# Kernel tuning notes

Measured on AMD Instinct MI355X. Metric: run time of the kernel, lower is better.

## Reference

```python
import jax, jax.numpy as jnp
import numpy as np

# Semantic hierarchy configuration (stand-in for semantic_softmax_processor)
GROUP_SIZES = [8192, 4096, 2048, 1024, 512, 256, 128, 64, 32, 16]
NORM_FACTORS = [0.1] * len(GROUP_SIZES)
TOPK_CAP = 500
TEMPERATURE = 1.0
TOTAL_CLASSES = sum(GROUP_SIZES)  # 16368
BATCH = 1024


def setup_inputs() -> dict:
    key = jax.random.key(0)
    k1, k2, k3 = jax.random.split(key, 3)
    logits = jax.random.normal(k1, (BATCH, TOTAL_CLASSES), dtype=jnp.float32)
    logits_teacher = jax.random.normal(k2, (BATCH, TOTAL_CLASSES), dtype=jnp.float32)
    targets = jax.random.randint(k3, (BATCH,), 0, TOTAL_CLASSES, dtype=jnp.int64)
    return {"logits": logits, "logits_teacher": logits_teacher, "targets": targets}


def _group_kd_loss(s_logits, t_logits, temperature):
    # s_logits, t_logits: [B, C_i] for one semantic group
    B, C = t_logits.shape
    k = min(C, TOPK_CAP)
    # teacher top-k classes (sorted, largest)
    t_top, t_idx = jax.lax.top_k(t_logits, k)                 # [B, k]
    s_top = jnp.take_along_axis(s_logits, t_idx, axis=1)      # [B, k]
    log_p = jax.nn.log_softmax(s_top / temperature, axis=1)   # student log-probs
    log_q = jax.nn.log_softmax(t_top / temperature, axis=1)   # teacher log-probs
    q = jnp.exp(log_q)
    # KL(q || p), reduction='batchmean'
    kl = jnp.sum(q * (log_q - log_p)) / B
    return kl * temperature * temperature


def reference(logits, logits_teacher, targets):
    # targets are converted to semantic targets in the original module but are
    # never used in the loss computation (dead code) -> no effect on output.
    del targets
    total = jnp.float32(0.0)
    offset = 0
    for gsize, norm in zip(GROUP_SIZES, NORM_FACTORS):
        s_i = jax.lax.slice_in_dim(logits, offset, offset + gsize, axis=1)
        t_i = jax.lax.slice_in_dim(logits_teacher, offset, offset + gsize, axis=1)
        total = total + _group_kd_loss(s_i, t_i, TEMPERATURE) * norm
        offset += gsize
    return total
```

## Files before the change

### kernel.cpp

```cpp
#include <hip/hip_runtime.h>
#include <stdint.h>
#include <float.h>

#define TOTAL 16368
#define KSEL 500
#define CAP 1280
#define NSLOT 20
#define HCAP 672
#define NSEG 21
#define NBUCKET 64

__device__ __forceinline__ uint32_t fkey(float f) {
    uint32_t u = __float_as_uint(f);
    return (u & 0x80000000u) ? ~u : (u | 0x80000000u);
}
__device__ __forceinline__ float keyf(uint32_t k) {
    uint32_t u = (k & 0x80000000u) ? (k & 0x7FFFFFFFu) : ~k;
    return __uint_as_float(u);
}
__device__ __forceinline__ int wave_sumi(int v) {
    #pragma unroll
    for (int o = 32; o > 0; o >>= 1) v += __shfl_xor(v, o, 64);
    return v;
}
__device__ __forceinline__ float wave_sumf(float v) {
    #pragma unroll
    for (int o = 32; o > 0; o >>= 1) v += __shfl_xor(v, o, 64);
    return v;
}
__device__ __forceinline__ float wave_maxf(float v) {
    #pragma unroll
    for (int o = 32; o > 0; o >>= 1) v = fmaxf(v, __shfl_xor(v, o, 64));
    return v;
}
__device__ __forceinline__ void lse_merge(float& m, float& l, float m2, float l2) {
    float M = fmaxf(m, m2);
    l = l * __expf(m - M) + l2 * __expf(m2 - M);
    m = M;
}

__device__ __noinline__ float wave_slow_kl(const float* __restrict__ t,
                                           const float* __restrict__ s, int C) {
    const int lane = threadIdx.x & 63;
    uint64_t lo = 0ull, hi = (1ull << 45), tau = 0ull;
    int cl = C, ch = 0;
    for (int it = 0; it < 100; ++it) {
        uint64_t span = hi - lo;
        if (span <= 1ull) { tau = lo; break; }
        uint64_t mid;
        if (it & 1) mid = lo + (span >> 1);
        else {
            uint64_t st = span * (uint64_t)(cl - KSEL) / (uint64_t)(cl - ch);
            if (st < 1) st = 1;
            if (st > span - 1) st = span - 1;
            mid = lo + st;
        }
        int c = 0;
        for (int i = lane; i < C; i += 64) {
            uint64_t ck = ((uint64_t)fkey(t[i]) << 13) | (uint64_t)(8191 - i);
            c += (ck > mid);
        }
        c = wave_sumi(c);
        if (c == KSEL) { tau = mid; break; }
        if (c > KSEL) { lo = mid; cl = c; } else { hi = mid; ch = c; }
    }
    float tmx = -FLT_MAX;
    for (int i = lane; i < C; i += 64) tmx = fmaxf(tmx, t[i]);
    tmx = wave_maxf(tmx);
    float St = 0.f, Stt = 0.f, Sts = 0.f, sm = -FLT_MAX;
    for (int i = lane; i < C; i += 64) {
        float x = t[i];
        uint64_t ck = ((uint64_t)fkey(x) << 13) | (uint64_t)(8191 - i);
        if (ck > tau) {
            float e = __expf(x - tmx), v = s[i];
            St += e; Stt += e * x; Sts += e * v;
            sm = fmaxf(sm, v);
        }
    }
    St = wave_sumf(St); Stt = wave_sumf(Stt); Sts = wave_sumf(Sts); sm = wave_maxf(sm);
    float Ss = 0.f;
    for (int i = lane; i < C; i += 64) {
        uint64_t ck = ((uint64_t)fkey(t[i]) << 13) | (uint64_t)(8191 - i);
        if (ck > tau) Ss += __expf(s[i] - sm);
    }
    Ss = wave_sumf(Ss);
    if (lane == 0)
        return (Stt - Sts) / St - tmx - __logf(St) + sm + __logf(Ss);
    return 0.f;
}

template <int NF4>
__device__ float big_wave(const float* __restrict__ tg, const float* __restrict__ s,
                          float thr, float* vals, uint16_t* idxs) {
    const int lane = threadIdx.x & 63;
    const float4* t4 = (const float4*)tg;
    int cnt = 0;
    #pragma unroll
    for (int c0 = 0; c0 < NF4; c0 += 8) {
        float4 buf[8];
        #pragma unroll
        for (int u = 0; u < 8; ++u) buf[u] = t4[(c0 + u) * 64 + lane];
        int myc = 0;
        #pragma unroll
        for (int u = 0; u < 8; ++u)
            myc += (buf[u].x > thr) + (buf[u].y > thr) +
                   (buf[u].z > thr) + (buf[u].w > thr);
        int inc = myc;
        #pragma unroll
        for (int o = 1; o < 64; o <<= 1) {
            int y = __shfl_up(inc, o, 64);
            if (lane >= o) inc += y;
        }
        int base = cnt + inc - myc;
        cnt += __shfl(inc, 63, 64);
        #pragma unroll
        for (int u = 0; u < 8; ++u) {
            float xs[4] = {buf[u].x, buf[u].y, buf[u].z, buf[u].w};
            #pragma unroll
            for (int q = 0; q < 4; ++q) {
                if (xs[q] > thr) {
                    if (base < CAP) {
                        vals[base] = xs[q];
                        idxs[base] = (uint16_t)((((c0 + u) * 64 + lane) << 2) + q);
                    }
                    ++base;
                }
            }
        }
    }
    if (cnt < KSEL || cnt > CAP) return wave_slow_kl(tg, s, NF4 * 256);

    uint32_t key[NSLOT];
    float svc[NSLOT];
    #pragma unroll
    for (int j = 0; j < NSLOT; ++j) {
        int p = lane + j * 64;
        bool v = p < cnt;
        key[j] = v ? fkey(vals[p]) : 0u;
        svc[j] = v ? s[(int)idxs[p]] : 0.f;
    }
    uint32_t kmx = 0u, kmn = 0xFFFFFFFFu;
    #pragma unroll
    for (int j = 0; j < NSLOT; ++j) {
        uint32_t k = key[j];
        kmx = k > kmx ? k : kmx;
        if (k) kmn = k < kmn ? k : kmn;
    }
    #pragma unroll
    for (int o = 32; o > 0; o >>= 1) {
        uint32_t a = __shfl_xor(kmx, o, 64); kmx = a > kmx ? a : kmx;
        uint32_t b = __shfl_xor(kmn, o, 64); kmn = b < kmn ? b : kmn;
    }
    const float tmax = keyf(kmx);

    uint32_t lo = kmn - 1u, hi = kmx, tauhi = kmx;
    int cl = cnt, ch = 0, cut = -1;
    bool exact = false;
    for (int it = 0; it < 80; ++it) {
        uint32_t span = hi - lo;
        if (span <= 1u) break;
        uint32_t mid;
        if (!(it & 1)) {
            uint64_t st = (uint64_t)span * (uint32_t)(cl - KSEL) / (uint32_t)(cl - ch);
            if (st < 1) st = 1;
            if (st > span - 1) st = span - 1;
            mid = lo + (uint32_t)st;
        } else mid = lo + (span >> 1);
        int c = 0;
        #pragma unroll
        for (int j = 0; j < NSLOT; ++j) c += (key[j] > mid);
        c = wave_sumi(c);
        if (c == KSEL) { tauhi = mid; exact = true; break; }
        if (c > KSEL) { lo = mid; cl = c; } else { hi = mid; ch = c; }
    }
    if (!exact) {
        tauhi = hi;
        const int nT = KSEL - ch, nTie = cl - ch;
        if (nT >= nTie) cut = 0x7FFFFFFF;
        else {
            int l = -1, h = 8191;
            while (h - l > 1) {
                int m = (l + h) >> 1;
                int c = 0;
                #pragma unroll
                for (int j = 0; j < NSLOT; ++j) {
                    int p = lane + j * 64;
                    c += (key[j] == tauhi && p < cnt && (int)idxs[p] <= m);
                }
                c = wave_sumi(c);
                if (c >= nT) h = m; else l = m;
            }
            cut = h;
        }
    }

    uint32_t selm = 0u;
    if (cut == -1) {
        #pragma unroll
        for (int j = 0; j < NSLOT; ++j) selm |= (key[j] > tauhi ? 1u : 0u) << j;
    } else if (cut == 0x7FFFFFFF) {
        #pragma unroll
        for (int j = 0; j < NSLOT; ++j) selm |= (key[j] >= tauhi ? 1u : 0u) << j;
    } else {
        #pragma unroll
        for (int j = 0; j < NSLOT; ++j) {
            int p = lane + j * 64;
            bool sj = (key[j] > tauhi) ||
                      (key[j] == tauhi && p < cnt && (int)idxs[p] <= cut);
            selm |= (sj ? 1u : 0u) << j;
        }
    }

    float St = 0.f, Stt = 0.f, Sts = 0.f, sm = -FLT_MAX;
    #pragma unroll
    for (int j = 0; j < NSLOT; ++j) {
        if (selm & (1u << j)) {
            float tv = keyf(key[j]);
            float e = __expf(tv - tmax);
            St += e; Stt += e * tv; Sts += e * svc[j];
            sm = fmaxf(sm, svc[j]);
        }
    }
    #pragma unroll
    for (int o = 32; o > 0; o >>= 1) {
        St  += __shfl_xor(St,  o, 64);
        Stt += __shfl_xor(Stt, o, 64);
        Sts += __shfl_xor(Sts, o, 64);
        sm = fmaxf(sm, __shfl_xor(sm, o, 64));
    }
    float Ss = 0.f;
    #pragma unroll
    for (int j = 0; j < NSLOT; ++j)
        if (selm & (1u << j)) Ss += __expf(svc[j] - sm);
    Ss = wave_sumf(Ss);
    if (lane == 0)
        return (Stt - Sts) / St - tmax - __logf(St) + sm + __logf(Ss);
    return 0.f;
}

__device__ int half_compact(const float* __restrict__ tq, const float* __restrict__ sg,
                            float thr, int idx_off,
                            uint32_t* kv, float* sv, uint16_t* ix) {
    const int lane = threadIdx.x & 63;
    const float4* t4 = (const float4*)tq;
    int cnt = 0;
    #pragma unroll
    for (int c0 = 0; c0 < 16; c0 += 8) {
        float4 buf[8];
        #pragma unroll
        for (int u = 0; u < 8; ++u) buf[u] = t4[(c0 + u) * 64 + lane];
        int myc = 0;
        #pragma unroll
        for (int u = 0; u < 8; ++u)
            myc += (buf[u].x > thr) + (buf[u].y > thr) +
                   (buf[u].z > thr) + (buf[u].w > thr);
        int inc = myc;
        #pragma unroll
        for (int o = 1; o < 64; o <<= 1) {
            int y = __shfl_up(inc, o, 64);
            if (lane >= o) inc += y;
        }
        int base = cnt + inc - myc;
        cnt += __shfl(inc, 63, 64);
        #pragma unroll
        for (int u = 0; u < 8; ++u) {
            float xs[4] = {buf[u].x, buf[u].y, buf[u].z, buf[u].w};
            #pragma unroll
            for (int q = 0; q < 4; ++q) {
                if (xs[q] > thr) {
                    if (base < HCAP) {
                        kv[base] = fkey(xs[q]);
                        ix[base] = (uint16_t)(((((c0 + u) * 64 + lane) << 2) + q)
                                              + idx_off);
                    }
                    ++base;
                }
            }
        }
    }
    if (cnt <= HCAP) {
        for (int p = cnt + lane; p < HCAP; p += 64) kv[p] = 0u;
        float r[11];
        #pragma unroll
        for (int j = 0; j < 11; ++j) {
            int p = lane + j * 64;
            r[j] = (p < cnt) ? sg[(int)ix[p]] : 0.f;
        }
        #pragma unroll
        for (int j = 0; j < 11; ++j) {
            int p = lane + j * 64;
            if (p < cnt) sv[p] = r[j];
        }
    }
    return cnt;
}

__device__ float pair_select(const uint32_t* __restrict__ kv,
                             const float* __restrict__ sv,
                             const uint16_t* __restrict__ ix,
                             const int* cnts,
                             const float* __restrict__ tg,
                             const float* __restrict__ sg) {
    const int lane = threadIdx.x & 63;
    const int tot = cnts[0] + cnts[1];
    bool bad = (tot < KSEL) || (cnts[0] > HCAP) || (cnts[1] > HCAP);
    if (bad) return wave_slow_kl(tg, sg, 8192);

    uint32_t key[NSEG];
    #pragma unroll
    for (int j = 0; j < NSEG; ++j) key[j] = kv[lane + j * 64];

    uint32_t kmx = 0u, kmn = 0xFFFFFFFFu;
    #pragma unroll
    for (int j = 0; j < NSEG; ++j) {
        uint32_t k = key[j];
        kmx = k > kmx ? k : kmx;
        if (k) kmn = k < kmn ? k : kmn;
    }
    #pragma unroll
    for (int o = 32; o > 0; o >>= 1) {
        uint32_t a = __shfl_xor(kmx, o, 64); kmx = a > kmx ? a : kmx;
        uint32_t b = __shfl_xor(kmn, o, 64); kmn = b < kmn ? b : kmn;
    }
    const float tmax = keyf(kmx);

    uint32_t lo = kmn - 1u, hi = kmx, tauhi = kmx;
    int cl = tot, ch = 0, cut = -1;
    bool exact = false;
    for (int it = 0; it < 80; ++it) {
        uint32_t span = hi - lo;
        if (span <= 1u) break;
        uint32_t mid;
        if (!(it & 1)) {
            uint64_t st = (uint64_t)span * (uint32_t)(cl - KSEL) / (uint32_t)(cl - ch);
            if (st < 1) st = 1;
            if (st > span - 1) st = span - 1;
            mid = lo + (uint32_t)st;
        } else mid = lo + (span >> 1);
        int c = 0;
        #pragma unroll
        for (int j = 0; j < NSEG; ++j) c += (key[j] > mid);
        c = wave_sumi(c);
        if (c == KSEL) { tauhi = mid; exact = true; break; }
        if (c > KSEL) { lo = mid; cl = c; } else { hi = mid; ch = c; }
    }
    if (!exact) {
        tauhi = hi;
        const int nT = KSEL - ch, nTie = cl - ch;
        if (nT >= nTie) cut = 0x7FFFFFFF;
        else {
            int l = -1, h = 8191;
            while (h - l > 1) {
                int m = (l + h) >> 1;
                int c = 0;
                #pragma unroll
                for (int j = 0; j < NSEG; ++j)
                    c += (key[j] == tauhi && (int)ix[lane + j * 64] <= m);
                c = wave_sumi(c);
                if (c >= nT) h = m; else l = m;
            }
            cut = h;
        }
    }

    uint32_t selm = 0u;
    if (cut == -1) {
        #pragma unroll
        for (int j = 0; j < NSEG; ++j) selm |= (key[j] > tauhi ? 1u : 0u) << j;
    } else if (cut == 0x7FFFFFFF) {
        #pragma unroll
        for (int j = 0; j < NSEG; ++j) selm |= (key[j] >= tauhi ? 1u : 0u) << j;
    } else {
        #pragma unroll
        for (int j = 0; j < NSEG; ++j) {
            bool sj = (key[j] > tauhi) ||
                      (key[j] == tauhi && (int)ix[lane + j * 64] <= cut);
            selm |= (sj ? 1u : 0u) << j;
        }
    }

    float St = 0.f, Stt = 0.f, Sts = 0.f, sm = -FLT_MAX;
    #pragma unroll
    for (int j = 0; j < NSEG; ++j) {
        if (selm & (1u << j)) {
            float tv = keyf(key[j]);
            float e = __expf(tv - tmax);
            float s = sv[lane + j * 64];
            St += e; Stt += e * tv; Sts += e * s;
            sm = fmaxf(sm, s);
        }
    }
    #pragma unroll
    for (int o = 32; o > 0; o >>= 1) {
        St  += __shfl_xor(St,  o, 64);
        Stt += __shfl_xor(Stt, o, 64);
        Sts += __shfl_xor(Sts, o, 64);
        sm = fmaxf(sm, __shfl_xor(sm, o, 64));
    }
    float Ss = 0.f;
    #pragma unroll
    for (int j = 0; j < NSEG; ++j)
        if (selm & (1u << j)) Ss += __expf(sv[lane + j * 64] - sm);
    Ss = wave_sumf(Ss);
    if (lane == 0)
        return (Stt - Sts) / St - tmax - __logf(St) + sm + __logf(Ss);
    return 0.f;
}

template <int NS, class IdxF>
__device__ float select_accum(uint32_t (&key)[NS], IdxF idxOf, const float* svp) {
    const int lane = threadIdx.x & 63;
    uint32_t kmx = 0u, kmn = 0xFFFFFFFFu;
    #pragma unroll
    for (int j = 0; j < NS; ++j) {
        uint32_t k = key[j];
        kmx = k > kmx ? k : kmx;
        kmn = k < kmn ? k : kmn;
    }
    #pragma unroll
    for (int o = 32; o > 0; o >>= 1) {
        uint32_t a = __shfl_xor(kmx, o, 64); kmx = a > kmx ? a : kmx;
        uint32_t b = __shfl_xor(kmn, o, 64); kmn = b < kmn ? b : kmn;
    }
    const float tmax = keyf(kmx);

    uint32_t lo = kmn - 1u, hi = kmx, tauhi = kmx;
    int cl = NS * 64, ch = 0, cut = -1;
    bool exact = false;
    for (int it = 0; it < 80; ++it) {
        uint32_t span = hi - lo;
        if (span <= 1u) break;
        uint32_t mid;
        if (!(it & 1)) {
            uint64_t st = (uint64_t)span * (uint32_t)(cl - KSEL) / (uint32_t)(cl - ch);
            if (st < 1) st = 1;
            if (st > span - 1) st = span - 1;
            mid = lo + (uint32_t)st;
        } else mid = lo + (span >> 1);
        int c = 0;
        #pragma unroll
        for (int j = 0; j < NS; ++j) c += (key[j] > mid);
        c = wave_sumi(c);
        if (c == KSEL) { tauhi = mid; exact = true; break; }
        if (c > KSEL) { lo = mid; cl = c; } else { hi = mid; ch = c; }
    }
    if (!exact) {
        tauhi = hi;
        const int nT = KSEL - ch, nTie = cl - ch;
        if (nT >= nTie) cut = 0x7FFFFFFF;
        else {
            int l = -1, h = NS * 64 - 1;
            while (h - l > 1) {
                int m = (l + h) >> 1;
                int c = 0;
                #pragma unroll
                for (int j = 0; j < NS; ++j)
                    c += (key[j] == tauhi && idxOf(j) <= m);
                c = wave_sumi(c);
                if (c >= nT) h = m; else l = m;
            }
            cut = h;
        }
    }

    float St = 0.f, Stt = 0.f, Sts = 0.f, sm = -FLT_MAX;
    #pragma unroll
    for (int j = 0; j < NS; ++j) {
        uint32_t kj = key[j];
        bool sj = (kj > tauhi) || (kj == tauhi && idxOf(j) <= cut);
        if (sj) {
            float tv = keyf(kj);
            float e = __expf(tv - tmax);
            St += e; Stt += e * tv; Sts += e * svp[j];
            sm = fmaxf(sm, svp[j]);
        }
    }
    #pragma unroll
    for (int o = 32; o > 0; o >>= 1) {
        St  += __shfl_xor(St,  o, 64);
        Stt += __shfl_xor(Stt, o, 64);
        Sts += __shfl_xor(Sts, o, 64);
        sm = fmaxf(sm, __shfl_xor(sm, o, 64));
    }
    float Ss = 0.f;
    #pragma unroll
    for (int j = 0; j < NS; ++j) {
        uint32_t kj = key[j];
        bool sj = (kj > tauhi) || (kj == tauhi && idxOf(j) <= cut);
        if (sj) Ss += __expf(svp[j] - sm);
    }
    Ss = wave_sumf(Ss);
    if (lane == 0)
        return (Stt - Sts) / St - tmax - __logf(St) + sm + __logf(Ss);
    return 0.f;
}

template <int NJ>
__device__ float mid_wave(const float* __restrict__ t, const float* __restrict__ s) {
    const int lane = threadIdx.x & 63;
    const float4* t4 = (const float4*)t;
    const float4* s4 = (const float4*)s;
    uint32_t key[NJ];
    float svp[NJ];
    #pragma unroll
    for (int c = 0; c < NJ / 4; ++c) {
        float4 x = t4[lane + c * 64];
        float4 y = s4[lane + c * 64];
        key[4 * c + 0] = fkey(x.x); key[4 * c + 1] = fkey(x.y);
        key[4 * c + 2] = fkey(x.z); key[4 * c + 3] = fkey(x.w);
        svp[4 * c + 0] = y.x; svp[4 * c + 1] = y.y;
        svp[4 * c + 2] = y.z; svp[4 * c + 3] = y.w;
    }
    auto idxOf = [&](int j) { return ((lane + (j >> 2) * 64) << 2) + (j & 3); };
    return select_accum<NJ>(key, idxOf, svp);
}

__device__ float tiny_group(const float* __restrict__ t, const float* __restrict__ s,
                            int Cg) {
    const int lane = threadIdx.x & 63;
    float St = 0.f, Stt = 0.f, Sts = 0.f, m = -FLT_MAX, l = 0.f;
    float tv[4], svv[4];
    #pragma unroll
    for (int q = 0; q < 4; ++q) {
        int i = lane + q * 64;
        bool va = i < Cg;
        tv[q] = va ? t[i] : -FLT_MAX;
        svv[q] = va ? s[i] : 0.f;
    }
    float mx = -FLT_MAX;
    #pragma unroll
    for (int q = 0; q < 4; ++q) mx = fmaxf(mx, tv[q]);
    mx = wave_maxf(mx);
    #pragma unroll
    for (int q = 0; q < 4; ++q) {
        if (lane + q * 64 < Cg) {
            float e = __expf(tv[q] - mx);
            St += e; Stt += e * tv[q]; Sts += e * svv[q];
            float x = svv[q];
            if (x > m) { l = l * __expf(m - x) + 1.f; m = x; }
            else       { l += __expf(x - m); }
        }
    }
    #pragma unroll
    for (int o = 32; o > 0; o >>= 1) {
        St  += __shfl_xor(St,  o, 64);
        Stt += __shfl_xor(Stt, o, 64);
        Sts += __shfl_xor(Sts, o, 64);
        float m2 = __shfl_xor(m, o, 64);
        float l2 = __shfl_xor(l, o, 64);
        lse_merge(m, l, m2, l2);
    }
    if (lane == 0)
        return (Stt - Sts) / St - mx - __logf(St) + m + __logf(l);
    return 0.f;
}

__global__ __launch_bounds__(256, 4) void kd_all(const float* __restrict__ sL,
                                                 const float* __restrict__ tL,
                                                 float* __restrict__ partial) {
    __shared__ uint32_t kv[2 * HCAP];
    __shared__ float    sv[2 * HCAP];
    __shared__ uint16_t ix[2 * HCAP];
    __shared__ int      cnts[2];
    __shared__ float    vals1[CAP];
    __shared__ uint16_t idxs1[CAP];

    const int row = blockIdx.x;
    const int w = threadIdx.x >> 6;
    const int lane = threadIdx.x & 63;
    const float* tr = tL + (size_t)row * TOTAL;
    const float* sr = sL + (size_t)row * TOTAL;

    float kl = 0.f;

    switch (w) {
    case 0: {
        int c = half_compact(tr, sr, 1.10f, 0, kv, sv, ix);
        if (lane == 0) cnts[0] = c;
        break;
    }
    case 1: {
        int c = half_compact(tr + 4096, sr, 1.10f, 4096,
                             kv + HCAP, sv + HCAP, ix + HCAP);
        if (lane == 0) cnts[1] = c;
        kl += tiny_group(tr + 15872, sr + 15872, 256);
        kl += tiny_group(tr + 16128, sr + 16128, 128);
        kl += tiny_group(tr + 16256, sr + 16256, 64);
        kl += tiny_group(tr + 16320, sr + 16320, 32);
        kl += tiny_group(tr + 16352, sr + 16352, 16);
        break;
    }
    case 2:
        kl  = big_wave<16>(tr + 8192, sr + 8192, 0.60f, vals1, idxs1);
        kl += mid_wave<8>(tr + 15360, sr + 15360);
        break;
    default:
        kl  = mid_wave<32>(tr + 12288, sr + 12288);
        kl += mid_wave<16>(tr + 14336, sr + 14336);
        break;
    }

    __syncthreads();

    if (w == 0)
        kl += pair_select(kv, sv, ix, cnts, tr, sr);

    if (lane == 0)
        atomicAdd(&partial[(row + w * 37) & (NBUCKET - 1)], kl * (0.1f / 1024.f));
}

__global__ void zero_ws(float* partial) {
    if (threadIdx.x < NBUCKET) partial[threadIdx.x] = 0.f;
}

__global__ void final_sum(const float* __restrict__ partial, float* __restrict__ out) {
    float v = (threadIdx.x < NBUCKET) ? partial[threadIdx.x] : 0.f;
    #pragma unroll
    for (int o = 32; o > 0; o >>= 1) v += __shfl_down(v, o, 64);
    if (threadIdx.x == 0) out[0] = v;
}

extern "C" void kernel_launch(void* const* d_in, const int* in_sizes, int n_in,
                              void* d_out, int out_size, void* d_ws, size_t ws_size,
                              hipStream_t stream) {
    (void)in_sizes; (void)n_in; (void)ws_size; (void)out_size;
    const float* s = (const float*)d_in[0];
    const float* t = (const float*)d_in[1];
    float* out = (float*)d_out;
    float* ws = (float*)d_ws;

    hipLaunchKernelGGL(zero_ws, dim3(1), dim3(64), 0, stream, ws);
    hipLaunchKernelGGL(kd_all, dim3(1024), dim3(256), 0, stream, s, t, ws);
    hipLaunchKernelGGL(final_sum, dim3(1), dim3(64), 0, stream, ws, out);
}
```

Measured before the change: 188.0 us.

## Split each row across two block types to rebalance per-wave work

The kernel now launches two blocks per row. Type A blocks split the 8192-class group across four waves, each compacting a quarter slice, then run a segmented select. Type B blocks split the 4096 group across two waves and handle the remaining groups on the other waves. Compaction switches from a shuffle prefix scan to ballot plus mbcnt ranks, and count reductions use ballot popcount. Binary-search loops are kept rolled and the occupancy hint is raised. The aim is to cut the critical path of the slowest wave in each row, at the cost of twice as many blocks, more fallback paths and more threshold-tuned capacity limits.

```diff
diff --git a/kernel.cpp b/kernel.cpp
--- a/kernel.cpp
+++ b/kernel.cpp
@@ -4,11 +4,20 @@
 
 #define TOTAL 16368
 #define KSEL 500
-#define CAP 1280
-#define NSLOT 20
-#define HCAP 672
-#define NSEG 21
+#define Q0CAP 384
+#define Q1CAP 704
+#define G2CAP 768
 #define NBUCKET 64
+
+#define A_KV 0
+#define A_SV 6144
+#define A_IX 12288
+#define B_KV 0
+#define B_SV 5632
+#define B_IX 11264
+#define B_G2V 14080
+#define B_G2I 17152
+#define SMEM_BYTES 18688
 
 __device__ __forceinline__ uint32_t fkey(float f) {
     uint32_t u = __float_as_uint(f);
@@ -17,6 +26,10 @@
 __device__ __forceinline__ float keyf(uint32_t k) {
     uint32_t u = (k & 0x80000000u) ? (k & 0x7FFFFFFFu) : ~k;
     return __uint_as_float(u);
+}
+__device__ __forceinline__ int lanerank(uint64_t m) {
+    return __builtin_amdgcn_mbcnt_hi((uint32_t)(m >> 32),
+           __builtin_amdgcn_mbcnt_lo((uint32_t)m, 0));
 }
 __device__ __forceinline__ int wave_sumi(int v) {
     #pragma unroll
@@ -44,6 +57,7 @@
     const int lane = threadIdx.x & 63;
     uint64_t lo = 0ull, hi = (1ull << 45), tau = 0ull;
     int cl = C, ch = 0;
+    #pragma unroll 1
     for (int it = 0; it < 100; ++it) {
         uint64_t span = hi - lo;
         if (span <= 1ull) { tau = lo; break; }
@@ -56,6 +70,7 @@
             mid = lo + st;
         }
         int c = 0;
+        #pragma unroll 1
         for (int i = lane; i < C; i += 64) {
             uint64_t ck = ((uint64_t)fkey(t[i]) << 13) | (uint64_t)(8191 - i);
             c += (ck > mid);
@@ -68,6 +83,7 @@
     for (int i = lane; i < C; i += 64) tmx = fmaxf(tmx, t[i]);
     tmx = wave_maxf(tmx);
     float St = 0.f, Stt = 0.f, Sts = 0.f, sm = -FLT_MAX;
+    #pragma unroll 1
     for (int i = lane; i < C; i += 64) {
         float x = t[i];
         uint64_t ck = ((uint64_t)fkey(x) << 13) | (uint64_t)(8191 - i);
@@ -79,6 +95,7 @@
     }
     St = wave_sumf(St); Stt = wave_sumf(Stt); Sts = wave_sumf(Sts); sm = wave_maxf(sm);
     float Ss = 0.f;
+    #pragma unroll 1
     for (int i = lane; i < C; i += 64) {
         uint64_t ck = ((uint64_t)fkey(t[i]) << 13) | (uint64_t)(8191 - i);
         if (ck > tau) Ss += __expf(s[i] - sm);
@@ -89,59 +106,76 @@
     return 0.f;
 }
 
-template <int NF4>
-__device__ float big_wave(const float* __restrict__ tg, const float* __restrict__ s,
-                          float thr, float* vals, uint16_t* idxs) {
-    const int lane = threadIdx.x & 63;
-    const float4* t4 = (const float4*)tg;
+template <int CAP>
+__device__ int slice_compact(const float* __restrict__ tq,
+                             const float* __restrict__ sg,
+                             float thr, int idx_off,
+                             uint32_t* kv, float* sv, uint16_t* ix) {
+    const int lane = threadIdx.x & 63;
+    const float4* t4 = (const float4*)tq;
+    float4 tb[8];
+    #pragma unroll
+    for (int u = 0; u < 8; ++u) tb[u] = t4[u * 64 + lane];
     int cnt = 0;
     #pragma unroll
-    for (int c0 = 0; c0 < NF4; c0 += 8) {
-        float4 buf[8];
-        #pragma unroll
-        for (int u = 0; u < 8; ++u) buf[u] = t4[(c0 + u) * 64 + lane];
-        int myc = 0;
-        #pragma unroll
-        for (int u = 0; u < 8; ++u)
-            myc += (buf[u].x > thr) + (buf[u].y > thr) +
-                   (buf[u].z > thr) + (buf[u].w > thr);
-        int inc = myc;
-        #pragma unroll
-        for (int o = 1; o < 64; o <<= 1) {
-            int y = __shfl_up(inc, o, 64);
-            if (lane >= o) inc += y;
-        }
-        int base = cnt + inc - myc;
-        cnt += __shfl(inc, 63, 64);
-        #pragma unroll
-        for (int u = 0; u < 8; ++u) {
-            float xs[4] = {buf[u].x, buf[u].y, buf[u].z, buf[u].w};
-            #pragma unroll
-            for (int q = 0; q < 4; ++q) {
-                if (xs[q] > thr) {
-                    if (base < CAP) {
-                        vals[base] = xs[q];
-                        idxs[base] = (uint16_t)((((c0 + u) * 64 + lane) << 2) + q);
-                    }
-                    ++base;
+    for (int u = 0; u < 8; ++u) {
+        float tx[4] = {tb[u].x, tb[u].y, tb[u].z, tb[u].w};
+        #pragma unroll
+        for (int q = 0; q < 4; ++q) {
+            bool p = tx[q] > thr;
+            uint64_t m = __ballot(p);
+            if (p) {
+                int ofs = cnt + lanerank(m);
+                if (ofs < CAP) {
+                    kv[ofs] = fkey(tx[q]);
+                    ix[ofs] = (uint16_t)((((u * 64 + lane) << 2) + q) + idx_off);
                 }
             }
-        }
-    }
-    if (cnt < KSEL || cnt > CAP) return wave_slow_kl(tg, s, NF4 * 256);
-
-    uint32_t key[NSLOT];
-    float svc[NSLOT];
-    #pragma unroll
-    for (int j = 0; j < NSLOT; ++j) {
-        int p = lane + j * 64;
-        bool v = p < cnt;
-        key[j] = v ? fkey(vals[p]) : 0u;
-        svc[j] = v ? s[(int)idxs[p]] : 0.f;
-    }
+            cnt += (int)__popcll(m);
+        }
+    }
+    if (cnt <= CAP) {
+        for (int p = cnt + lane; p < CAP; p += 64) kv[p] = 0u;
+        constexpr int NR = CAP / 64;
+        float r[NR];
+        #pragma unroll
+        for (int j = 0; j < NR; ++j) {
+            int p = lane + j * 64;
+            r[j] = (p < cnt) ? sg[(int)ix[p]] : 0.f;
+        }
+        #pragma unroll
+        for (int j = 0; j < NR; ++j) {
+            int p = lane + j * 64;
+            if (p < cnt) sv[p] = r[j];
+        }
+    }
+    return cnt;
+}
+
+template <int S, int SEGCAP, int NS>
+__device__ float seg_select(const uint32_t* __restrict__ kv,
+                            const float* __restrict__ sv,
+                            const uint16_t* __restrict__ ix,
+                            const int* __restrict__ cnts, int C,
+                            const float* __restrict__ tg,
+                            const float* __restrict__ sg) {
+    const int lane = threadIdx.x & 63;
+    int tot = 0; bool bad = false;
+    #pragma unroll
+    for (int q = 0; q < S; ++q) {
+        int c = cnts[q];
+        tot += c;
+        bad = bad || (c > SEGCAP);
+    }
+    if (bad || tot < KSEL) return wave_slow_kl(tg, sg, C);
+
+    uint32_t key[NS];
+    #pragma unroll
+    for (int j = 0; j < NS; ++j) key[j] = kv[lane + j * 64];
+
     uint32_t kmx = 0u, kmn = 0xFFFFFFFFu;
     #pragma unroll
-    for (int j = 0; j < NSLOT; ++j) {
+    for (int j = 0; j < NS; ++j) {
         uint32_t k = key[j];
         kmx = k > kmx ? k : kmx;
         if (k) kmn = k < kmn ? k : kmn;
@@ -154,8 +188,9 @@
     const float tmax = keyf(kmx);
 
     uint32_t lo = kmn - 1u, hi = kmx, tauhi = kmx;
-    int cl = cnt, ch = 0, cut = -1;
+    int cl = tot, ch = 0, cut = -1;
     bool exact = false;
+    #pragma unroll 1
     for (int it = 0; it < 80; ++it) {
         uint32_t span = hi - lo;
         if (span <= 1u) break;
@@ -168,8 +203,8 @@
         } else mid = lo + (span >> 1);
         int c = 0;
         #pragma unroll
-        for (int j = 0; j < NSLOT; ++j) c += (key[j] > mid);
-        c = wave_sumi(c);
+        for (int j = 0; j < NS; ++j)
+            c += (int)__popcll(__ballot(key[j] > mid));
         if (c == KSEL) { tauhi = mid; exact = true; break; }
         if (c > KSEL) { lo = mid; cl = c; } else { hi = mid; ch = c; }
     }
@@ -178,16 +213,15 @@
         const int nT = KSEL - ch, nTie = cl - ch;
         if (nT >= nTie) cut = 0x7FFFFFFF;
         else {
-            int l = -1, h = 8191;
+            int l = -1, h = C - 1;
+            #pragma unroll 1
             while (h - l > 1) {
                 int m = (l + h) >> 1;
                 int c = 0;
                 #pragma unroll
-                for (int j = 0; j < NSLOT; ++j) {
-                    int p = lane + j * 64;
-                    c += (key[j] == tauhi && p < cnt && (int)idxs[p] <= m);
-                }
-                c = wave_sumi(c);
+                for (int j = 0; j < NS; ++j)
+                    c += (int)__popcll(__ballot(key[j] == tauhi &&
+                                                (int)ix[lane + j * 64] <= m));
                 if (c >= nT) h = m; else l = m;
             }
             cut = h;
@@ -197,28 +231,28 @@
     uint32_t selm = 0u;
     if (cut == -1) {
         #pragma unroll
-        for (int j = 0; j < NSLOT; ++j) selm |= (key[j] > tauhi ? 1u : 0u) << j;
+        for (int j = 0; j < NS; ++j) selm |= (key[j] > tauhi ? 1u : 0u) << j;
     } else if (cut == 0x7FFFFFFF) {
         #pragma unroll
-        for (int j = 0; j < NSLOT; ++j) selm |= (key[j] >= tauhi ? 1u : 0u) << j;
+        for (int j = 0; j < NS; ++j) selm |= (key[j] >= tauhi ? 1u : 0u) << j;
     } else {
         #pragma unroll
-        for (int j = 0; j < NSLOT; ++j) {
-            int p = lane + j * 64;
+        for (int j = 0; j < NS; ++j) {
             bool sj = (key[j] > tauhi) ||
-                      (key[j] == tauhi && p < cnt && (int)idxs[p] <= cut);
+                      (key[j] == tauhi && (int)ix[lane + j * 64] <= cut);
             selm |= (sj ? 1u : 0u) << j;
         }
     }
 
     float St = 0.f, Stt = 0.f, Sts = 0.f, sm = -FLT_MAX;
     #pragma unroll
-    for (int j = 0; j < NSLOT; ++j) {
+    for (int j = 0; j < NS; ++j) {
         if (selm & (1u << j)) {
             float tv = keyf(key[j]);
             float e = __expf(tv - tmax);
-            St += e; Stt += e * tv; Sts += e * svc[j];
-            sm = fmaxf(sm, svc[j]);
+            float s = sv[lane + j * 64];
+            St += e; Stt += e * tv; Sts += e * s;
+            sm = fmaxf(sm, s);
         }
     }
     #pragma unroll
@@ -230,89 +264,64 @@
     }
     float Ss = 0.f;
     #pragma unroll
-    for (int j = 0; j < NSLOT; ++j)
-        if (selm & (1u << j)) Ss += __expf(svc[j] - sm);
+    for (int j = 0; j < NS; ++j)
+        if (selm & (1u << j)) Ss += __expf(sv[lane + j * 64] - sm);
     Ss = wave_sumf(Ss);
     if (lane == 0)
         return (Stt - Sts) / St - tmax - __logf(St) + sm + __logf(Ss);
     return 0.f;
 }
 
-__device__ int half_compact(const float* __restrict__ tq, const float* __restrict__ sg,
-                            float thr, int idx_off,
-                            uint32_t* kv, float* sv, uint16_t* ix) {
-    const int lane = threadIdx.x & 63;
-    const float4* t4 = (const float4*)tq;
+template <int NF4, int CAPT, int NST>
+__device__ float big_wave(const float* __restrict__ tg, const float* __restrict__ s,
+                          float thr, float* vals, uint16_t* idxs) {
+    const int lane = threadIdx.x & 63;
+    const float4* t4 = (const float4*)tg;
+    constexpr int NB = NF4 / 8;
     int cnt = 0;
-    #pragma unroll
-    for (int c0 = 0; c0 < 16; c0 += 8) {
-        float4 buf[8];
-        #pragma unroll
-        for (int u = 0; u < 8; ++u) buf[u] = t4[(c0 + u) * 64 + lane];
-        int myc = 0;
-        #pragma unroll
-        for (int u = 0; u < 8; ++u)
-            myc += (buf[u].x > thr) + (buf[u].y > thr) +
-                   (buf[u].z > thr) + (buf[u].w > thr);
-        int inc = myc;
-        #pragma unroll
-        for (int o = 1; o < 64; o <<= 1) {
-            int y = __shfl_up(inc, o, 64);
-            if (lane >= o) inc += y;
-        }
-        int base = cnt + inc - myc;
-        cnt += __shfl(inc, 63, 64);
+    float4 buf[8], nxt[8];
+    #pragma unroll
+    for (int u = 0; u < 8; ++u) buf[u] = t4[u * 64 + lane];
+    #pragma unroll 1
+    for (int b = 0; b < NB; ++b) {
+        if (b + 1 < NB) {
+            #pragma unroll
+            for (int u = 0; u < 8; ++u)
+                nxt[u] = t4[((b + 1) * 8 + u) * 64 + lane];
+        }
         #pragma unroll
         for (int u = 0; u < 8; ++u) {
             float xs[4] = {buf[u].x, buf[u].y, buf[u].z, buf[u].w};
             #pragma unroll
             for (int q = 0; q < 4; ++q) {
-                if (xs[q] > thr) {
-                    if (base < HCAP) {
-                        kv[base] = fkey(xs[q]);
-                        ix[base] = (uint16_t)(((((c0 + u) * 64 + lane) << 2) + q)
-                                              + idx_off);
+                bool p = xs[q] > thr;
+                uint64_t m = __ballot(p);
+                if (p) {
+                    int ofs = cnt + lanerank(m);
+                    if (ofs < CAPT) {
+                        vals[ofs] = xs[q];
+                        idxs[ofs] = (uint16_t)((((b * 8 + u) * 64 + lane) << 2) + q);
                     }
-                    ++base;
                 }
+                cnt += (int)__popcll(m);
             }
         }
-    }
-    if (cnt <= HCAP) {
-        for (int p = cnt + lane; p < HCAP; p += 64) kv[p] = 0u;
-        float r[11];
-        #pragma unroll
-        for (int j = 0; j < 11; ++j) {
-            int p = lane + j * 64;
-            r[j] = (p < cnt) ? sg[(int)ix[p]] : 0.f;
-        }
-        #pragma unroll
-        for (int j = 0; j < 11; ++j) {
-            int p = lane + j * 64;
-            if (p < cnt) sv[p] = r[j];
-        }
-    }
-    return cnt;
-}
-
-__device__ float pair_select(const uint32_t* __restrict__ kv,
-                             const float* __restrict__ sv,
-                             const uint16_t* __restrict__ ix,
-                             const int* cnts,
-                             const float* __restrict__ tg,
-                             const float* __restrict__ sg) {
-    const int lane = threadIdx.x & 63;
-    const int tot = cnts[0] + cnts[1];
-    bool bad = (tot < KSEL) || (cnts[0] > HCAP) || (cnts[1] > HCAP);
-    if (bad) return wave_slow_kl(tg, sg, 8192);
-
-    uint32_t key[NSEG];
-    #pragma unroll
-    for (int j = 0; j < NSEG; ++j) key[j] = kv[lane + j * 64];
-
+        if (b + 1 < NB) {
+            #pragma unroll
+            for (int u = 0; u < 8; ++u) buf[u] = nxt[u];
+        }
+    }
+    if (cnt < KSEL || cnt > CAPT) return wave_slow_kl(tg, s, NF4 * 256);
+
+    uint32_t key[NST];
+    #pragma unroll
+    for (int j = 0; j < NST; ++j) {
+        int p = lane + j * 64;
+        key[j] = (p < cnt) ? fkey(vals[p]) : 0u;
+    }
     uint32_t kmx = 0u, kmn = 0xFFFFFFFFu;
     #pragma unroll
-    for (int j = 0; j < NSEG; ++j) {
+    for (int j = 0; j < NST; ++j) {
         uint32_t k = key[j];
         kmx = k > kmx ? k : kmx;
         if (k) kmn = k < kmn ? k : kmn;
@@ -320,13 +329,14 @@
     #pragma unroll
     for (int o = 32; o > 0; o >>= 1) {
         uint32_t a = __shfl_xor(kmx, o, 64); kmx = a > kmx ? a : kmx;
-        uint32_t b = __shfl_xor(kmn, o, 64); kmn = b < kmn ? b : kmn;
+        uint32_t b2 = __shfl_xor(kmn, o, 64); kmn = b2 < kmn ? b2 : kmn;
     }
     const float tmax = keyf(kmx);
 
     uint32_t lo = kmn - 1u, hi = kmx, tauhi = kmx;
-    int cl = tot, ch = 0, cut = -1;
+    int cl = cnt, ch = 0, cut = -1;
     bool exact = false;
+    #pragma unroll 1
     for (int it = 0; it < 80; ++it) {
         uint32_t span = hi - lo;
         if (span <= 1u) break;
@@ -339,8 +349,8 @@
         } else mid = lo + (span >> 1);
         int c = 0;
         #pragma unroll
-        for (int j = 0; j < NSEG; ++j) c += (key[j] > mid);
-        c = wave_sumi(c);
+        for (int j = 0; j < NST; ++j)
+            c += (int)__popcll(__ballot(key[j] > mid));
         if (c == KSEL) { tauhi = mid; exact = true; break; }
         if (c > KSEL) { lo = mid; cl = c; } else { hi = mid; ch = c; }
     }
@@ -349,14 +359,20 @@
         const int nT = KSEL - ch, nTie = cl - ch;
         if (nT >= nTie) cut = 0x7FFFFFFF;
         else {
+            int idxr[NST];
+            #pragma unroll
+            for (int j = 0; j < NST; ++j) {
+                int p = lane + j * 64;
+                idxr[j] = (p < cnt) ? (int)idxs[p] : 0x7FFF;
+            }
             int l = -1, h = 8191;
+            #pragma unroll 1
             while (h - l > 1) {
                 int m = (l + h) >> 1;
                 int c = 0;
                 #pragma unroll
-                for (int j = 0; j < NSEG; ++j)
-                    c += (key[j] == tauhi && (int)ix[lane + j * 64] <= m);
-                c = wave_sumi(c);
+                for (int j = 0; j < NST; ++j)
+                    c += (int)__popcll(__ballot(key[j] == tauhi && idxr[j] <= m));
                 if (c >= nT) h = m; else l = m;
             }
             cut = h;
@@ -366,28 +382,33 @@
     uint32_t selm = 0u;
     if (cut == -1) {
         #pragma unroll
-        for (int j = 0; j < NSEG; ++j) selm |= (key[j] > tauhi ? 1u : 0u) << j;
+        for (int j = 0; j < NST; ++j) selm |= (key[j] > tauhi ? 1u : 0u) << j;
     } else if (cut == 0x7FFFFFFF) {
         #pragma unroll
-        for (int j = 0; j < NSEG; ++j) selm |= (key[j] >= tauhi ? 1u : 0u) << j;
+        for (int j = 0; j < NST; ++j) selm |= (key[j] >= tauhi ? 1u : 0u) << j;
     } else {
         #pragma unroll
-        for (int j = 0; j < NSEG; ++j) {
+        for (int j = 0; j < NST; ++j) {
+            int p = lane + j * 64;
             bool sj = (key[j] > tauhi) ||
-                      (key[j] == tauhi && (int)ix[lane + j * 64] <= cut);
+                      (key[j] == tauhi && p < cnt && (int)idxs[p] <= cut);
             selm |= (sj ? 1u : 0u) << j;
         }
     }
 
+    float svc[NST];
+    #pragma unroll
+    for (int j = 0; j < NST; ++j)
+        svc[j] = (selm & (1u << j)) ? s[(int)idxs[lane + j * 64]] : 0.f;
+
     float St = 0.f, Stt = 0.f, Sts = 0.f, sm = -FLT_MAX;
     #pragma unroll
-    for (int j = 0; j < NSEG; ++j) {
+    for (int j = 0; j < NST; ++j) {
         if (selm & (1u << j)) {
             float tv = keyf(key[j]);
             float e = __expf(tv - tmax);
-            float s = sv[lane + j * 64];
-            St += e; Stt += e * tv; Sts += e * s;
-            sm = fmaxf(sm, s);
+            St += e; Stt += e * tv; Sts += e * svc[j];
+            sm = fmaxf(sm, svc[j]);
         }
     }
     #pragma unroll
@@ -399,8 +420,8 @@
     }
     float Ss = 0.f;
     #pragma unroll
-    for (int j = 0; j < NSEG; ++j)
-        if (selm & (1u << j)) Ss += __expf(sv[lane + j * 64] - sm);
+    for (int j = 0; j < NST; ++j)
+        if (selm & (1u << j)) Ss += __expf(svc[j] - sm);
     Ss = wave_sumf(Ss);
     if (lane == 0)
         return (Stt - Sts) / St - tmax - __logf(St) + sm + __logf(Ss);
@@ -427,6 +448,7 @@
     uint32_t lo = kmn - 1u, hi = kmx, tauhi = kmx;
     int cl = NS * 64, ch = 0, cut = -1;
     bool exact = false;
+    #pragma unroll 1
     for (int it = 0; it < 80; ++it) {
         uint32_t span = hi - lo;
         if (span <= 1u) break;
@@ -439,8 +461,8 @@
         } else mid = lo + (span >> 1);
         int c = 0;
         #pragma unroll
-        for (int j = 0; j < NS; ++j) c += (key[j] > mid);
-        c = wave_sumi(c);
+        for (int j = 0; j < NS; ++j)
+            c += (int)__popcll(__ballot(key[j] > mid));
         if (c == KSEL) { tauhi = mid; exact = true; break; }
         if (c > KSEL) { lo = mid; cl = c; } else { hi = mid; ch = c; }
     }
@@ -450,13 +472,13 @@
         if (nT >= nTie) cut = 0x7FFFFFFF;
         else {
             int l = -1, h = NS * 64 - 1;
+            #pragma unroll 1
             while (h - l > 1) {
                 int m = (l + h) >> 1;
                 int c = 0;
                 #pragma unroll
                 for (int j = 0; j < NS; ++j)
-                    c += (key[j] == tauhi && idxOf(j) <= m);
-                c = wave_sumi(c);
+                    c += (int)__popcll(__ballot(key[j] == tauhi && idxOf(j) <= m));
                 if (c >= nT) h = m; else l = m;
             }
             cut = h;
@@ -555,58 +577,71 @@
     return 0.f;
 }
 
-__global__ __launch_bounds__(256, 4) void kd_all(const float* __restrict__ sL,
-                                                 const float* __restrict__ tL,
-                                                 float* __restrict__ partial) {
-    __shared__ uint32_t kv[2 * HCAP];
-    __shared__ float    sv[2 * HCAP];
-    __shared__ uint16_t ix[2 * HCAP];
-    __shared__ int      cnts[2];
-    __shared__ float    vals1[CAP];
-    __shared__ uint16_t idxs1[CAP];
-
-    const int row = blockIdx.x;
+__global__ __launch_bounds__(256, 6) void kd_coop(const float* __restrict__ sL,
+                                                  const float* __restrict__ tL,
+                                                  float* __restrict__ partial) {
+    __shared__ char smem[SMEM_BYTES] __attribute__((aligned(16)));
+    __shared__ int cnts[4];
+    const int bid = blockIdx.x;
     const int w = threadIdx.x >> 6;
     const int lane = threadIdx.x & 63;
+    const bool typeA = bid < 1024;
+    const int row = typeA ? bid : bid - 1024;
     const float* tr = tL + (size_t)row * TOTAL;
     const float* sr = sL + (size_t)row * TOTAL;
 
     float kl = 0.f;
 
-    switch (w) {
-    case 0: {
-        int c = half_compact(tr, sr, 1.10f, 0, kv, sv, ix);
-        if (lane == 0) cnts[0] = c;
-        break;
-    }
-    case 1: {
-        int c = half_compact(tr + 4096, sr, 1.10f, 4096,
-                             kv + HCAP, sv + HCAP, ix + HCAP);
-        if (lane == 0) cnts[1] = c;
-        kl += tiny_group(tr + 15872, sr + 15872, 256);
-        kl += tiny_group(tr + 16128, sr + 16128, 128);
-        kl += tiny_group(tr + 16256, sr + 16256, 64);
-        kl += tiny_group(tr + 16320, sr + 16320, 32);
-        kl += tiny_group(tr + 16352, sr + 16352, 16);
-        break;
-    }
-    case 2:
-        kl  = big_wave<16>(tr + 8192, sr + 8192, 0.60f, vals1, idxs1);
-        kl += mid_wave<8>(tr + 15360, sr + 15360);
-        break;
-    default:
-        kl  = mid_wave<32>(tr + 12288, sr + 12288);
-        kl += mid_wave<16>(tr + 14336, sr + 14336);
-        break;
+    if (typeA) {
+        uint32_t* kv = (uint32_t*)(smem + A_KV);
+        float*    sv = (float*)(smem + A_SV);
+        uint16_t* ix = (uint16_t*)(smem + A_IX);
+        int c = slice_compact<Q0CAP>(tr + w * 2048, sr, 1.10f, w * 2048,
+                                     kv + w * Q0CAP, sv + w * Q0CAP, ix + w * Q0CAP);
+        if (lane == 0) cnts[w] = c;
+    } else {
+        if (w < 2) {
+            uint32_t* kv = (uint32_t*)(smem + B_KV);
+            float*    sv = (float*)(smem + B_SV);
+            uint16_t* ix = (uint16_t*)(smem + B_IX);
+            int c = slice_compact<Q1CAP>(tr + 8192 + w * 2048, sr + 8192, 0.60f,
+                                         w * 2048,
+                                         kv + w * Q1CAP, sv + w * Q1CAP,
+                                         ix + w * Q1CAP);
+            if (lane == 0) cnts[w] = c;
+        } else if (w == 2) {
+            float*    g2v = (float*)(smem + B_G2V);
+            uint16_t* g2i = (uint16_t*)(smem + B_G2I);
+            kl = big_wave<8, G2CAP, 12>(tr + 12288, sr + 12288, 0.50f, g2v, g2i);
+        } else {
+            kl  = mid_wave<16>(tr + 14336, sr + 14336);
+            kl += mid_wave<8>(tr + 15360, sr + 15360);
+            kl += tiny_group(tr + 15872, sr + 15872, 256);
+            kl += tiny_group(tr + 16128, sr + 16128, 128);
+            kl += tiny_group(tr + 16256, sr + 16256, 64);
+            kl += tiny_group(tr + 16320, sr + 16320, 32);
+            kl += tiny_group(tr + 16352, sr + 16352, 16);
+        }
     }
 
     __syncthreads();
 
-    if (w == 0)
-        kl += pair_select(kv, sv, ix, cnts, tr, sr);
+    if (w == 0) {
+        if (typeA)
+            kl += seg_select<4, Q0CAP, 24>((uint32_t*)(smem + A_KV),
+                                           (float*)(smem + A_SV),
+                                           (uint16_t*)(smem + A_IX),
+                                           cnts, 8192, tr, sr);
+        else
+            kl += seg_select<2, Q1CAP, 22>((uint32_t*)(smem + B_KV),
+                                           (float*)(smem + B_SV),
+                                           (uint16_t*)(smem + B_IX),
+                                           cnts, 4096, tr + 8192, sr + 8192);
+    }
 
     if (lane == 0)
-        atomicAdd(&partial[(row + w * 37) & (NBUCKET - 1)], kl * (0.1f / 1024.f));
+        atomicAdd(&partial[(row + w * 16 + (typeA ? 0 : 8)) & (NBUCKET - 1)],
+                  kl * (0.1f / 1024.f));
 }
 
 __global__ void zero_ws(float* partial) {
@@ -630,6 +665,6 @@
     float* ws = (float*)d_ws;
 
     hipLaunchKernelGGL(zero_ws, dim3(1), dim3(64), 0, stream, ws);
-    hipLaunchKernelGGL(kd_all, dim3(1024), dim3(256), 0, stream, s, t, ws);
+    hipLaunchKernelGGL(kd_coop, dim3(2048), dim3(256), 0, stream, s, t, ws);
     hipLaunchKernelGGL(final_sum, dim3(1), dim3(64), 0, stream, ws, out);
 }
```

After: 184.5 us. No clear change (-1.9%).
